# Optimization experiments

Hardware: AMD Instinct MI355X
Metric: run time of the kernel (lower is better)

The kernel has to match this reference:

```python
import jax, jax.numpy as jnp
import numpy as np
import math

N, E = 10000, 640000
IN, HID, OUT, EF = 64, 64, 64, 16


def setup_inputs() -> dict:
    key = jax.random.key(0)
    ks = jax.random.split(key, 16)
    def lin(k, fan_in, fan_out):
        return jax.random.normal(k, (fan_in, fan_out), jnp.float32) / np.sqrt(fan_in)
    return {
        "node_feat": jax.random.normal(ks[0], (N, IN), jnp.float32),
        "coord_feat": jax.random.normal(ks[1], (N, 3), jnp.float32),
        "edge_feat": jax.random.normal(ks[2], (E, EF), jnp.float32),
        "W_e1": lin(ks[3], 2 * IN + EF + 1, HID), "b_e1": jnp.zeros((HID,), jnp.float32),
        "W_e2": lin(ks[4], HID, HID), "b_e2": jnp.zeros((HID,), jnp.float32),
        "W_n1": lin(ks[5], IN + HID, HID), "b_n1": jnp.zeros((HID,), jnp.float32),
        "W_n2": lin(ks[6], HID, OUT), "b_n2": jnp.zeros((OUT,), jnp.float32),
        "W_q": lin(ks[7], IN, HID),
        "W_k": lin(ks[8], IN + EF + 1, HID),
        "src": jax.random.randint(ks[9], (E,), 0, N, jnp.int32),
        "dst": jax.random.randint(ks[10], (E,), 0, N, jnp.int32),
    }


def reference(node_feat, coord_feat, edge_feat,
              W_e1, b_e1, W_e2, b_e2, W_n1, b_n1, W_n2, b_n2,
              W_q, W_k, src, dst):
    silu = jax.nn.silu
    # per-edge gathers
    h_src = node_feat[src]                      # [E, IN]
    h_dst = node_feat[dst]                      # [E, IN]
    x_diff = coord_feat[src] - coord_feat[dst]  # [E, 3]
    dist = jnp.sqrt(jnp.sum(x_diff * x_diff, axis=1, keepdims=True))  # [E, 1]
    # edge MLP message
    f = jnp.concatenate([h_src, h_dst, dist, edge_feat], axis=-1)      # [E, 2*IN+1+EF]
    msg_h = silu(silu(f @ W_e1 + b_e1) @ W_e2 + b_e2)                  # [E, HID]
    # attention score (QK dot)
    k_raw = jnp.concatenate([h_src, dist, edge_feat], axis=-1)         # [E, IN+1+EF]
    msg_k = k_raw @ W_k                                                # [E, HID]
    msg_q = h_dst @ W_q                                                # [E, HID]
    e = jnp.sum(msg_k * msg_q, axis=-1) / math.sqrt(HID)               # [E]
    # segment softmax over incoming edges of each dst node
    e_max = jax.ops.segment_max(e, dst, num_segments=N)                # [N]
    e_exp = jnp.exp(e - e_max[dst])                                    # [E]
    denom = jax.ops.segment_sum(e_exp, dst, num_segments=N)            # [N]
    att = e_exp / denom[dst]                                           # [E]
    # attention-weighted scatter-sum aggregation
    h_neigh = jax.ops.segment_sum(msg_h * att[:, None], dst, num_segments=N)  # [N, HID]
    # node MLP
    h = silu(jnp.concatenate([node_feat, h_neigh], axis=-1) @ W_n1 + b_n1) @ W_n2 + b_n2
    return h
```

## Files before the change

kernel.cpp:

```cpp
#include <hip/hip_runtime.h>

#define NN 10000
#define NE 640000

typedef __attribute__((ext_vector_type(8))) short bf16x8;
typedef __attribute__((ext_vector_type(4))) short s16x4;
typedef __attribute__((ext_vector_type(4))) float f32x4;

#define MFMA __builtin_amdgcn_mfma_f32_16x16x32_bf16

static __device__ __forceinline__ float silu_f(float x) {
    return x / (1.f + __expf(-x));
}
static __device__ __forceinline__ float silu_fast(float x) {
    float d = 1.f + __expf(-x);
    float r; asm("v_rcp_f32 %0, %1" : "=v"(r) : "v"(d));
    return x * r;
}
static __device__ __forceinline__ short f2bf(float x) {
    union { float f; unsigned u; } v; v.f = x;
    unsigned r = (v.u + 0x7FFF + ((v.u >> 16) & 1)) >> 16;
    return (short)r;
}
static __device__ __forceinline__ float bf2f(short h) {
    union { float f; unsigned u; } v; v.u = ((unsigned)(unsigned short)h) << 16;
    return v.f;
}

__global__ __launch_bounds__(256) void k_hist(const int* __restrict__ dst,
                                              int* __restrict__ cnt) {
    int e = blockIdx.x * 256 + threadIdx.x;
    if (e < NE) atomicAdd(&cnt[dst[e]], 1);
}

__global__ __launch_bounds__(256) void k_scan(const int* __restrict__ cnt,
                                              int* __restrict__ row_start,
                                              int* __restrict__ cursor) {
    __shared__ int sv[NN];
    __shared__ int part[256];
    __shared__ int base[257];
    const int t = threadIdx.x;
    for (int i = t; i < NN; i += 256) sv[i] = cnt[i];
    __syncthreads();
    int s = 0;
    #pragma unroll
    for (int i = 0; i < 40; i++) {
        int idx = t * 40 + i;
        int v = (idx < NN) ? sv[idx] : 0;
        if (idx < NN) sv[idx] = s;
        s += v;
    }
    part[t] = s;
    __syncthreads();
    if (t == 0) {
        int a = 0;
        for (int j = 0; j < 256; j++) { base[j] = a; a += part[j]; }
        base[256] = a;
    }
    __syncthreads();
    for (int i = t; i < NN; i += 256) {
        int v = base[i / 40] + sv[i];
        row_start[i] = v; cursor[i] = v;
    }
    if (t == 0) row_start[NN] = base[256];
}

__global__ __launch_bounds__(256) void k_scatter(const int* __restrict__ dst,
                                                 int* __restrict__ cursor,
                                                 int* __restrict__ perm) {
    int e = blockIdx.x * 256 + threadIdx.x;
    if (e < NE) {
        int d = dst[e];
        int p = atomicAdd(&cursor[d], 1);
        perm[p] = e;
    }
}

__global__ __launch_bounds__(256) void k_pack(
    const int* __restrict__ perm, const int* __restrict__ src,
    const int* __restrict__ dst, const float* __restrict__ ef,
    const float* __restrict__ coord,
    int* __restrict__ src_s, unsigned short* __restrict__ dist_s,
    unsigned short* __restrict__ efs)
{
    int p = blockIdx.x * 256 + threadIdx.x;
    if (p >= NE) return;
    const int e = perm[p];
    const int s = src[e];
    const int d = dst[e];

    const float dx = coord[s*3+0] - coord[d*3+0];
    const float dy = coord[s*3+1] - coord[d*3+1];
    const float dz = coord[s*3+2] - coord[d*3+2];
    const float dist = sqrtf(dx*dx + dy*dy + dz*dz);

    src_s[p] = s;
    dist_s[p] = (unsigned short)f2bf(dist);

    const float4* ep = (const float4*)(ef + (size_t)e*16);
    #pragma unroll
    for (int j = 0; j < 4; j++) {
        float4 a = ep[j];
        s16x4 p4;
        p4[0] = f2bf(a.x); p4[1] = f2bf(a.y); p4[2] = f2bf(a.z); p4[3] = f2bf(a.w);
        *(s16x4*)&efs[(size_t)p*16 + j*4] = p4;
    }
}

__global__ __launch_bounds__(256) void node_pre_kernel(
    const float* __restrict__ node_feat,
    const float* __restrict__ W_e1,
    const float* __restrict__ W_k,
    const float* __restrict__ W_q,
    short* __restrict__ nfb, float* __restrict__ B,
    float* __restrict__ G, float* __restrict__ EQn, float* __restrict__ WQn)
{
    __shared__ float sW1b[64*64];
    __shared__ float sWq[64*64];
    __shared__ float sWk[64*65];
    __shared__ float sWke[16*65];
    __shared__ __align__(16) float sx[4][64];
    __shared__ __align__(16) float sq[4][64];

    for (int i = threadIdx.x; i < 64*64; i += 256) {
        sW1b[i] = W_e1[64*64 + i];
        sWq[i]  = W_q[i];
        int c = i >> 6, j = i & 63;
        sWk[c*65 + j] = W_k[i];
    }
    for (int i = threadIdx.x; i < 16*64; i += 256) {
        int k = i >> 6, j = i & 63;
        sWke[k*65 + j] = W_k[(65 + k)*64 + j];
    }
    __syncthreads();

    const int wid = threadIdx.x >> 6;
    const int lane = threadIdx.x & 63;
    for (int n = blockIdx.x * 4 + wid; n < NN; n += gridDim.x * 4) {
        float x = node_feat[n*64 + lane];
        nfb[n*64 + lane] = f2bf(x);
        sx[wid][lane] = x;
        float b = 0.f, q = 0.f;
        #pragma unroll
        for (int i = 0; i < 64; i += 4) {
            float4 x4 = *(const float4*)&sx[wid][i];
            b += x4.x*sW1b[(i+0)*64+lane] + x4.y*sW1b[(i+1)*64+lane]
               + x4.z*sW1b[(i+2)*64+lane] + x4.w*sW1b[(i+3)*64+lane];
            q += x4.x*sWq[(i+0)*64+lane] + x4.y*sWq[(i+1)*64+lane]
               + x4.z*sWq[(i+2)*64+lane] + x4.w*sWq[(i+3)*64+lane];
        }
        B[n*64 + lane] = b;
        sq[wid][lane] = q;

        float g = 0.f;
        #pragma unroll
        for (int j = 0; j < 64; j += 4) {
            float4 q4 = *(const float4*)&sq[wid][j];
            g += q4.x*sWk[lane*65 + j]   + q4.y*sWk[lane*65 + j+1]
               + q4.z*sWk[lane*65 + j+2] + q4.w*sWk[lane*65 + j+3];
        }
        G[n*64 + lane] = g;

        float p = W_k[64*64 + lane] * q;
        #pragma unroll
        for (int off = 32; off; off >>= 1) p += __shfl_xor(p, off);
        if (lane == 0) WQn[n] = p;

        int kk = lane & 15, pp = lane >> 4;
        float s = 0.f;
        #pragma unroll
        for (int jj = 0; jj < 16; jj++) {
            int j = pp*16 + jj;
            s += sWke[kk*65 + j] * sq[wid][j];
        }
        s += __shfl_xor(s, 16); s += __shfl_xor(s, 32);
        if (lane < 16) EQn[n*16 + kk] = s;
    }
}

__global__ __launch_bounds__(512, 2) void edge_kernel(
    const short* __restrict__ nfb, const int* __restrict__ src_s,
    const unsigned short* __restrict__ dist_s,
    const unsigned short* __restrict__ efs, const int* __restrict__ row_start,
    const float* __restrict__ W_e1, const float* __restrict__ b_e1,
    const float* __restrict__ W_e2, const float* __restrict__ b_e2,
    const float* __restrict__ B, const float* __restrict__ G,
    const float* __restrict__ EQn, const float* __restrict__ WQn,
    float* __restrict__ hout)
{
    __shared__ short sW1T[64*104];
    __shared__ short sW2T[64*72];
    __shared__ short sX[8][16*104];
    __shared__ short sH1[8][16*72];
    __shared__ __align__(16) float sG[8][64];
    __shared__ __align__(16) float sEQ[8][16];

    const int tid = threadIdx.x;
    const int wid = tid >> 6, l = tid & 63;
    const int cl = l & 15, rg = l >> 4;
    const int er = l >> 2, q = l & 3;

    for (int i = tid; i < 64*104; i += 512) sW1T[i] = 0;
    __syncthreads();
    for (int i = tid; i < 64*82; i += 512) {
        int k = i >> 6, c = i & 63;
        float v;
        if (k < 64)       v = W_e1[k*64 + c];
        else if (k < 80)  v = W_e1[(129 + k - 64)*64 + c];
        else if (k == 80) v = W_e1[128*64 + c];
        else              v = b_e1[c];
        int s = (c & 3) * 16 + (c >> 2);
        sW1T[s*104 + k] = f2bf(v);
    }
    for (int i = tid; i < 64*64; i += 512) {
        int k = i >> 6, c = i & 63;
        int s = (c & 3) * 16 + (c >> 2);
        sW2T[s*72 + k] = f2bf(W_e2[k*64 + c]);
    }
    if (l < 16) {
        #pragma unroll
        for (int c = 82; c < 96; c++) sX[wid][l*104 + c] = 0;
        sX[wid][l*104 + 81] = (short)0x3F80;
    }
    __syncthreads();

    const int n = blockIdx.x * 8 + wid;
    const int beg = row_start[n], end = row_start[n+1];

    const size_t nb = (size_t)n*64;
    const float4 Bb4 = *(const float4*)&B[nb + cl*4];
    const float4 b24 = *(const float4*)&b_e2[cl*4];
    sG[wid][l] = G[nb + l];
    if (l < 16) sEQ[wid][l] = EQn[(size_t)n*16 + l];
    const float wq = WQn[n];

    float hs0 = 0.f, hs1 = 0.f, hs2 = 0.f, hs3 = 0.f, den = 0.f;

    int idx = beg + er; if (idx > NE-1) idx = NE-1;
    int sN = src_s[idx];
    bf16x8 nfAN = *(const bf16x8*)&nfb[(size_t)sN*64 + q*8];
    bf16x8 nfBN = *(const bf16x8*)&nfb[(size_t)sN*64 + 32 + q*8];
    s16x4  efN  = *(const s16x4*)&efs[(size_t)idx*16 + q*4];
    unsigned short dN = dist_s[idx];

    for (int c0 = beg; c0 < end; c0 += 16) {
        bf16x8 nfA = nfAN, nfB = nfBN; s16x4 ef4 = efN;
        unsigned short dcur = dN;

        int idx2 = c0 + 16 + er; if (idx2 > NE-1) idx2 = NE-1;
        sN = src_s[idx2];
        nfAN = *(const bf16x8*)&nfb[(size_t)sN*64 + q*8];
        nfBN = *(const bf16x8*)&nfb[(size_t)sN*64 + 32 + q*8];
        efN  = *(const s16x4*)&efs[(size_t)idx2*16 + q*4];
        dN   = dist_s[idx2];

        const float dist = bf2f((short)dcur);
        float p_ = 0.f;
        #pragma unroll
        for (int i = 0; i < 8; i++) {
            p_ += bf2f(nfA[i]) * sG[wid][q*8 + i];
            p_ += bf2f(nfB[i]) * sG[wid][32 + q*8 + i];
        }
        #pragma unroll
        for (int i = 0; i < 4; i++)
            p_ += bf2f(ef4[i]) * sEQ[wid][q*4 + i];
        p_ += __shfl_xor(p_, 1); p_ += __shfl_xor(p_, 2);
        const float wgt = __expf((p_ + dist * wq) * 0.125f);

        *(bf16x8*)&sX[wid][er*104 + q*8]      = nfA;
        *(bf16x8*)&sX[wid][er*104 + 32 + q*8] = nfB;
        *(s16x4*)&sX[wid][er*104 + 64 + q*4]  = ef4;
        if (q == 0) sX[wid][er*104 + 80] = (short)dcur;

        bf16x8 ax0 = *(const bf16x8*)&sX[wid][cl*104 +  0 + rg*8];
        bf16x8 ax1 = *(const bf16x8*)&sX[wid][cl*104 + 32 + rg*8];
        bf16x8 ax2 = *(const bf16x8*)&sX[wid][cl*104 + 64 + rg*8];
        f32x4 a0 = {Bb4.x,Bb4.x,Bb4.x,Bb4.x}, a1 = {Bb4.y,Bb4.y,Bb4.y,Bb4.y};
        f32x4 a2 = {Bb4.z,Bb4.z,Bb4.z,Bb4.z}, a3 = {Bb4.w,Bb4.w,Bb4.w,Bb4.w};
        a0 = MFMA(ax0, *(const bf16x8*)&sW1T[( 0+cl)*104 +  0 + rg*8], a0, 0,0,0);
        a0 = MFMA(ax1, *(const bf16x8*)&sW1T[( 0+cl)*104 + 32 + rg*8], a0, 0,0,0);
        a0 = MFMA(ax2, *(const bf16x8*)&sW1T[( 0+cl)*104 + 64 + rg*8], a0, 0,0,0);
        a1 = MFMA(ax0, *(const bf16x8*)&sW1T[(16+cl)*104 +  0 + rg*8], a1, 0,0,0);
        a1 = MFMA(ax1, *(const bf16x8*)&sW1T[(16+cl)*104 + 32 + rg*8], a1, 0,0,0);
        a1 = MFMA(ax2, *(const bf16x8*)&sW1T[(16+cl)*104 + 64 + rg*8], a1, 0,0,0);
        a2 = MFMA(ax0, *(const bf16x8*)&sW1T[(32+cl)*104 +  0 + rg*8], a2, 0,0,0);
        a2 = MFMA(ax1, *(const bf16x8*)&sW1T[(32+cl)*104 + 32 + rg*8], a2, 0,0,0);
        a2 = MFMA(ax2, *(const bf16x8*)&sW1T[(32+cl)*104 + 64 + rg*8], a2, 0,0,0);
        a3 = MFMA(ax0, *(const bf16x8*)&sW1T[(48+cl)*104 +  0 + rg*8], a3, 0,0,0);
        a3 = MFMA(ax1, *(const bf16x8*)&sW1T[(48+cl)*104 + 32 + rg*8], a3, 0,0,0);
        a3 = MFMA(ax2, *(const bf16x8*)&sW1T[(48+cl)*104 + 64 + rg*8], a3, 0,0,0);
        #pragma unroll
        for (int r = 0; r < 4; r++) {
            int row = rg*4 + r;
            float s0 = silu_fast(a0[r]), s1 = silu_fast(a1[r]);
            float s2 = silu_fast(a2[r]), s3 = silu_fast(a3[r]);
            unsigned lo, hi;
            asm("v_cvt_pk_bf16_f32 %0, %1, %2" : "=v"(lo) : "v"(s0), "v"(s1));
            asm("v_cvt_pk_bf16_f32 %0, %1, %2" : "=v"(hi) : "v"(s2), "v"(s3));
            uint2 u; u.x = lo; u.y = hi;
            *(uint2*)&sH1[wid][row*72 + cl*4] = u;
        }

        bf16x8 ah0 = *(const bf16x8*)&sH1[wid][cl*72 + rg*8];
        bf16x8 ah1 = *(const bf16x8*)&sH1[wid][cl*72 + 32 + rg*8];
        f32x4 c0v = {b24.x,b24.x,b24.x,b24.x}, c1v = {b24.y,b24.y,b24.y,b24.y};
        f32x4 c2v = {b24.z,b24.z,b24.z,b24.z}, c3v = {b24.w,b24.w,b24.w,b24.w};
        c0v = MFMA(ah0, *(const bf16x8*)&sW2T[( 0+cl)*72 +      rg*8], c0v, 0,0,0);
        c0v = MFMA(ah1, *(const bf16x8*)&sW2T[( 0+cl)*72 + 32 + rg*8], c0v, 0,0,0);
        c1v = MFMA(ah0, *(const bf16x8*)&sW2T[(16+cl)*72 +      rg*8], c1v, 0,0,0);
        c1v = MFMA(ah1, *(const bf16x8*)&sW2T[(16+cl)*72 + 32 + rg*8], c1v, 0,0,0);
        c2v = MFMA(ah0, *(const bf16x8*)&sW2T[(32+cl)*72 +      rg*8], c2v, 0,0,0);
        c2v = MFMA(ah1, *(const bf16x8*)&sW2T[(32+cl)*72 + 32 + rg*8], c2v, 0,0,0);
        c3v = MFMA(ah0, *(const bf16x8*)&sW2T[(48+cl)*72 +      rg*8], c3v, 0,0,0);
        c3v = MFMA(ah1, *(const bf16x8*)&sW2T[(48+cl)*72 + 32 + rg*8], c3v, 0,0,0);

        #pragma unroll
        for (int r = 0; r < 4; r++) {
            int row = rg*4 + r;
            float wr = (c0 + row < end) ? __shfl(wgt, row << 2) : 0.f;
            hs0 += wr * silu_fast(c0v[r]);
            hs1 += wr * silu_fast(c1v[r]);
            hs2 += wr * silu_fast(c2v[r]);
            hs3 += wr * silu_fast(c3v[r]);
            den += wr;
        }
    }

    hs0 += __shfl_xor(hs0, 16); hs0 += __shfl_xor(hs0, 32);
    hs1 += __shfl_xor(hs1, 16); hs1 += __shfl_xor(hs1, 32);
    hs2 += __shfl_xor(hs2, 16); hs2 += __shfl_xor(hs2, 32);
    hs3 += __shfl_xor(hs3, 16); hs3 += __shfl_xor(hs3, 32);
    den += __shfl_xor(den, 16); den += __shfl_xor(den, 32);

    float v = (rg == 0) ? hs0 : (rg == 1) ? hs1 : (rg == 2) ? hs2 : hs3;
    hout[nb + cl*4 + rg] = (den > 0.f) ? v / den : 0.f;
}

__global__ __launch_bounds__(256) void node_out_kernel(
    const float* __restrict__ node_feat,
    const float* __restrict__ W_n1, const float* __restrict__ b_n1,
    const float* __restrict__ W_n2, const float* __restrict__ b_n2,
    const float* __restrict__ hacc, float* __restrict__ out)
{
    __shared__ float sWn1[128*64];
    __shared__ float sWn2[64*64];
    __shared__ __align__(16) float sx[4][64], sg[4][64], st[4][64];

    for (int i = threadIdx.x; i < 128*64; i += 256) sWn1[i] = W_n1[i];
    for (int i = threadIdx.x; i < 64*64; i += 256)  sWn2[i] = W_n2[i];
    __syncthreads();

    const int wid = threadIdx.x >> 6;
    const int lane = threadIdx.x & 63;
    for (int n = blockIdx.x * 4 + wid; n < NN; n += gridDim.x * 4) {
        sx[wid][lane] = node_feat[n*64 + lane];
        sg[wid][lane] = hacc[n*64 + lane];

        float acc = b_n1[lane];
        #pragma unroll
        for (int i = 0; i < 64; i += 4) {
            float4 x4 = *(const float4*)&sx[wid][i];
            float4 g4 = *(const float4*)&sg[wid][i];
            acc += x4.x*sWn1[(i+0)*64+lane] + x4.y*sWn1[(i+1)*64+lane]
                 + x4.z*sWn1[(i+2)*64+lane] + x4.w*sWn1[(i+3)*64+lane];
            acc += g4.x*sWn1[(64+i+0)*64+lane] + g4.y*sWn1[(64+i+1)*64+lane]
                 + g4.z*sWn1[(64+i+2)*64+lane] + g4.w*sWn1[(64+i+3)*64+lane];
        }
        const float tt = silu_f(acc);
        st[wid][lane] = tt;

        float acc2 = b_n2[lane];
        #pragma unroll
        for (int i = 0; i < 64; i += 4) {
            float4 t4 = *(const float4*)&st[wid][i];
            acc2 += t4.x*sWn2[(i+0)*64+lane] + t4.y*sWn2[(i+1)*64+lane]
                  + t4.z*sWn2[(i+2)*64+lane] + t4.w*sWn2[(i+3)*64+lane];
        }
        out[n*64 + lane] = acc2;
    }
}

extern "C" void kernel_launch(void* const* d_in, const int* in_sizes, int n_in,
                              void* d_out, int out_size, void* d_ws, size_t ws_size,
                              hipStream_t stream) {
    const float* node_feat = (const float*)d_in[0];
    const float* coord     = (const float*)d_in[1];
    const float* edge_feat = (const float*)d_in[2];
    const float* W_e1 = (const float*)d_in[3];
    const float* b_e1 = (const float*)d_in[4];
    const float* W_e2 = (const float*)d_in[5];
    const float* b_e2 = (const float*)d_in[6];
    const float* W_n1 = (const float*)d_in[7];
    const float* b_n1 = (const float*)d_in[8];
    const float* W_n2 = (const float*)d_in[9];
    const float* b_n2 = (const float*)d_in[10];
    const float* W_q  = (const float*)d_in[11];
    const float* W_k  = (const float*)d_in[12];
    const int* src = (const int*)d_in[13];
    const int* dst = (const int*)d_in[14];
    float* out = (float*)d_out;

    float* ws = (float*)d_ws;
    short* nfb       = (short*)ws;
    float* B         = ws + 320000;
    float* G         = ws + 960000;
    float* EQn       = ws + 1600000;
    float* WQn       = ws + 1760000;
    int*   cnt       = (int*)(ws + 1770000);
    int*   row_start = (int*)(ws + 1780000);
    int*   cursor    = (int*)(ws + 1790004);
    int*   perm      = (int*)(ws + 1800004);
    int*   src_s     = (int*)(ws + 2440004);
    unsigned short* dist_s = (unsigned short*)(ws + 3080004);
    unsigned short* efs    = (unsigned short*)(ws + 3400004);
    float* hacc      = ws + 8520004;

    hipMemsetAsync(cnt, 0, NN * sizeof(int), stream);

    node_pre_kernel<<<2500, 256, 0, stream>>>(node_feat, W_e1, W_k, W_q,
                                              nfb, B, G, EQn, WQn);
    k_hist<<<2500, 256, 0, stream>>>(dst, cnt);
    k_scan<<<1, 256, 0, stream>>>(cnt, row_start, cursor);
    k_scatter<<<2500, 256, 0, stream>>>(dst, cursor, perm);
    k_pack<<<2500, 256, 0, stream>>>(perm, src, dst, edge_feat, coord,
                                     src_s, dist_s, efs);
    edge_kernel<<<1250, 512, 0, stream>>>(nfb, src_s, dist_s, efs, row_start,
                                          W_e1, b_e1, W_e2, b_e2,
                                          B, G, EQn, WQn, hacc);
    node_out_kernel<<<2500, 256, 0, stream>>>(node_feat, W_n1, b_n1, W_n2, b_n2,
                                              hacc, out);
}
```

Baseline: 348.2 us.

## Feed gathered edge operands straight to MFMA and pipeline the two MLP layers

The edge kernel no longer stages gathered node and edge features through an LDS buffer. Each lane loads its slice directly in the MFMA operand layout, and the attention dot product now uses the same registers. The second MLP layer for the previous 16-edge chunk runs alongside the first layer of the current chunk, with the hidden tile carried in LDS and one extra drain iteration. The kernel also becomes a persistent grid-stride loop over nodes, with a higher occupancy hint and smaller grids for several kernels. This cuts LDS traffic and exposes overlap, at the cost of more registers and a risk that the smaller grids for the other kernels only work if those kernels loop over nodes.

```diff
diff --git a/kernel.cpp b/kernel.cpp
--- a/kernel.cpp
+++ b/kernel.cpp
@@ -178,7 +178,7 @@
     }
 }
 
-__global__ __launch_bounds__(512, 2) void edge_kernel(
+__global__ __launch_bounds__(512, 4) void edge_kernel(
     const short* __restrict__ nfb, const int* __restrict__ src_s,
     const unsigned short* __restrict__ dist_s,
     const unsigned short* __restrict__ efs, const int* __restrict__ row_start,
@@ -190,15 +190,12 @@
 {
     __shared__ short sW1T[64*104];
     __shared__ short sW2T[64*72];
-    __shared__ short sX[8][16*104];
     __shared__ short sH1[8][16*72];
-    __shared__ __align__(16) float sG[8][64];
-    __shared__ __align__(16) float sEQ[8][16];
+    __shared__ __align__(16) float sC[8][96];
 
     const int tid = threadIdx.x;
     const int wid = tid >> 6, l = tid & 63;
     const int cl = l & 15, rg = l >> 4;
-    const int er = l >> 2, q = l & 3;
 
     for (int i = tid; i < 64*104; i += 512) sW1T[i] = 0;
     __syncthreads();
@@ -217,123 +214,133 @@
         int s = (c & 3) * 16 + (c >> 2);
         sW2T[s*72 + k] = f2bf(W_e2[k*64 + c]);
     }
-    if (l < 16) {
-        #pragma unroll
-        for (int c = 82; c < 96; c++) sX[wid][l*104 + c] = 0;
-        sX[wid][l*104 + 81] = (short)0x3F80;
-    }
-    __syncthreads();
-
-    const int n = blockIdx.x * 8 + wid;
-    const int beg = row_start[n], end = row_start[n+1];
-
-    const size_t nb = (size_t)n*64;
-    const float4 Bb4 = *(const float4*)&B[nb + cl*4];
+    __syncthreads();
+
     const float4 b24 = *(const float4*)&b_e2[cl*4];
-    sG[wid][l] = G[nb + l];
-    if (l < 16) sEQ[wid][l] = EQn[(size_t)n*16 + l];
-    const float wq = WQn[n];
-
-    float hs0 = 0.f, hs1 = 0.f, hs2 = 0.f, hs3 = 0.f, den = 0.f;
-
-    int idx = beg + er; if (idx > NE-1) idx = NE-1;
-    int sN = src_s[idx];
-    bf16x8 nfAN = *(const bf16x8*)&nfb[(size_t)sN*64 + q*8];
-    bf16x8 nfBN = *(const bf16x8*)&nfb[(size_t)sN*64 + 32 + q*8];
-    s16x4  efN  = *(const s16x4*)&efs[(size_t)idx*16 + q*4];
-    unsigned short dN = dist_s[idx];
-
-    for (int c0 = beg; c0 < end; c0 += 16) {
-        bf16x8 nfA = nfAN, nfB = nfBN; s16x4 ef4 = efN;
-        unsigned short dcur = dN;
-
-        int idx2 = c0 + 16 + er; if (idx2 > NE-1) idx2 = NE-1;
-        sN = src_s[idx2];
-        nfAN = *(const bf16x8*)&nfb[(size_t)sN*64 + q*8];
-        nfBN = *(const bf16x8*)&nfb[(size_t)sN*64 + 32 + q*8];
-        efN  = *(const s16x4*)&efs[(size_t)idx2*16 + q*4];
-        dN   = dist_s[idx2];
-
-        const float dist = bf2f((short)dcur);
-        float p_ = 0.f;
-        #pragma unroll
-        for (int i = 0; i < 8; i++) {
-            p_ += bf2f(nfA[i]) * sG[wid][q*8 + i];
-            p_ += bf2f(nfB[i]) * sG[wid][32 + q*8 + i];
-        }
-        #pragma unroll
-        for (int i = 0; i < 4; i++)
-            p_ += bf2f(ef4[i]) * sEQ[wid][q*4 + i];
-        p_ += __shfl_xor(p_, 1); p_ += __shfl_xor(p_, 2);
-        const float wgt = __expf((p_ + dist * wq) * 0.125f);
-
-        *(bf16x8*)&sX[wid][er*104 + q*8]      = nfA;
-        *(bf16x8*)&sX[wid][er*104 + 32 + q*8] = nfB;
-        *(s16x4*)&sX[wid][er*104 + 64 + q*4]  = ef4;
-        if (q == 0) sX[wid][er*104 + 80] = (short)dcur;
-
-        bf16x8 ax0 = *(const bf16x8*)&sX[wid][cl*104 +  0 + rg*8];
-        bf16x8 ax1 = *(const bf16x8*)&sX[wid][cl*104 + 32 + rg*8];
-        bf16x8 ax2 = *(const bf16x8*)&sX[wid][cl*104 + 64 + rg*8];
-        f32x4 a0 = {Bb4.x,Bb4.x,Bb4.x,Bb4.x}, a1 = {Bb4.y,Bb4.y,Bb4.y,Bb4.y};
-        f32x4 a2 = {Bb4.z,Bb4.z,Bb4.z,Bb4.z}, a3 = {Bb4.w,Bb4.w,Bb4.w,Bb4.w};
-        a0 = MFMA(ax0, *(const bf16x8*)&sW1T[( 0+cl)*104 +  0 + rg*8], a0, 0,0,0);
-        a0 = MFMA(ax1, *(const bf16x8*)&sW1T[( 0+cl)*104 + 32 + rg*8], a0, 0,0,0);
-        a0 = MFMA(ax2, *(const bf16x8*)&sW1T[( 0+cl)*104 + 64 + rg*8], a0, 0,0,0);
-        a1 = MFMA(ax0, *(const bf16x8*)&sW1T[(16+cl)*104 +  0 + rg*8], a1, 0,0,0);
-        a1 = MFMA(ax1, *(const bf16x8*)&sW1T[(16+cl)*104 + 32 + rg*8], a1, 0,0,0);
-        a1 = MFMA(ax2, *(const bf16x8*)&sW1T[(16+cl)*104 + 64 + rg*8], a1, 0,0,0);
-        a2 = MFMA(ax0, *(const bf16x8*)&sW1T[(32+cl)*104 +  0 + rg*8], a2, 0,0,0);
-        a2 = MFMA(ax1, *(const bf16x8*)&sW1T[(32+cl)*104 + 32 + rg*8], a2, 0,0,0);
-        a2 = MFMA(ax2, *(const bf16x8*)&sW1T[(32+cl)*104 + 64 + rg*8], a2, 0,0,0);
-        a3 = MFMA(ax0, *(const bf16x8*)&sW1T[(48+cl)*104 +  0 + rg*8], a3, 0,0,0);
-        a3 = MFMA(ax1, *(const bf16x8*)&sW1T[(48+cl)*104 + 32 + rg*8], a3, 0,0,0);
-        a3 = MFMA(ax2, *(const bf16x8*)&sW1T[(48+cl)*104 + 64 + rg*8], a3, 0,0,0);
-        #pragma unroll
-        for (int r = 0; r < 4; r++) {
-            int row = rg*4 + r;
-            float s0 = silu_fast(a0[r]), s1 = silu_fast(a1[r]);
-            float s2 = silu_fast(a2[r]), s3 = silu_fast(a3[r]);
-            unsigned lo, hi;
-            asm("v_cvt_pk_bf16_f32 %0, %1, %2" : "=v"(lo) : "v"(s0), "v"(s1));
-            asm("v_cvt_pk_bf16_f32 %0, %1, %2" : "=v"(hi) : "v"(s2), "v"(s3));
-            uint2 u; u.x = lo; u.y = hi;
-            *(uint2*)&sH1[wid][row*72 + cl*4] = u;
-        }
-
-        bf16x8 ah0 = *(const bf16x8*)&sH1[wid][cl*72 + rg*8];
-        bf16x8 ah1 = *(const bf16x8*)&sH1[wid][cl*72 + 32 + rg*8];
-        f32x4 c0v = {b24.x,b24.x,b24.x,b24.x}, c1v = {b24.y,b24.y,b24.y,b24.y};
-        f32x4 c2v = {b24.z,b24.z,b24.z,b24.z}, c3v = {b24.w,b24.w,b24.w,b24.w};
-        c0v = MFMA(ah0, *(const bf16x8*)&sW2T[( 0+cl)*72 +      rg*8], c0v, 0,0,0);
-        c0v = MFMA(ah1, *(const bf16x8*)&sW2T[( 0+cl)*72 + 32 + rg*8], c0v, 0,0,0);
-        c1v = MFMA(ah0, *(const bf16x8*)&sW2T[(16+cl)*72 +      rg*8], c1v, 0,0,0);
-        c1v = MFMA(ah1, *(const bf16x8*)&sW2T[(16+cl)*72 + 32 + rg*8], c1v, 0,0,0);
-        c2v = MFMA(ah0, *(const bf16x8*)&sW2T[(32+cl)*72 +      rg*8], c2v, 0,0,0);
-        c2v = MFMA(ah1, *(const bf16x8*)&sW2T[(32+cl)*72 + 32 + rg*8], c2v, 0,0,0);
-        c3v = MFMA(ah0, *(const bf16x8*)&sW2T[(48+cl)*72 +      rg*8], c3v, 0,0,0);
-        c3v = MFMA(ah1, *(const bf16x8*)&sW2T[(48+cl)*72 + 32 + rg*8], c3v, 0,0,0);
-
-        #pragma unroll
-        for (int r = 0; r < 4; r++) {
-            int row = rg*4 + r;
-            float wr = (c0 + row < end) ? __shfl(wgt, row << 2) : 0.f;
-            hs0 += wr * silu_fast(c0v[r]);
-            hs1 += wr * silu_fast(c1v[r]);
-            hs2 += wr * silu_fast(c2v[r]);
-            hs3 += wr * silu_fast(c3v[r]);
-            den += wr;
-        }
-    }
-
-    hs0 += __shfl_xor(hs0, 16); hs0 += __shfl_xor(hs0, 32);
-    hs1 += __shfl_xor(hs1, 16); hs1 += __shfl_xor(hs1, 32);
-    hs2 += __shfl_xor(hs2, 16); hs2 += __shfl_xor(hs2, 32);
-    hs3 += __shfl_xor(hs3, 16); hs3 += __shfl_xor(hs3, 32);
-    den += __shfl_xor(den, 16); den += __shfl_xor(den, 32);
-
-    float v = (rg == 0) ? hs0 : (rg == 1) ? hs1 : (rg == 2) ? hs2 : hs3;
-    hout[nb + cl*4 + rg] = (den > 0.f) ? v / den : 0.f;
+
+    for (int n = blockIdx.x * 8 + wid; n < NN; n += gridDim.x * 8) {
+        const int beg = row_start[n], end = row_start[n+1];
+        const size_t nb = (size_t)n*64;
+        const float4 Bb4 = *(const float4*)&B[nb + cl*4];
+
+        sC[wid][l] = G[nb + l];
+        if (l < 16) sC[wid][64 + l] = EQn[(size_t)n*16 + l];
+        if (l == 16) sC[wid][80] = WQn[n];
+        if (l >= 17 && l < 32) sC[wid][64 + l] = 0.f;
+
+        {
+            unsigned* hp = (unsigned*)&sH1[wid][0];
+            #pragma unroll
+            for (int i = l; i < 576; i += 64) hp[i] = 0u;
+        }
+
+        float hs0 = 0.f, hs1 = 0.f, hs2 = 0.f, hs3 = 0.f, den = 0.f;
+        float w_prev = 0.f;
+
+        bf16x8 pA, pB, pE;
+        #pragma unroll
+        for (int i = 0; i < 8; i++) pE[i] = 0;
+        unsigned short pD = 0;
+        {
+            int idx = beg + cl; if (idx > NE-1) idx = NE-1;
+            int sN = src_s[idx];
+            pA = *(const bf16x8*)&nfb[(size_t)sN*64 + rg*8];
+            pB = *(const bf16x8*)&nfb[(size_t)sN*64 + 32 + rg*8];
+            if (rg < 2)       pE = *(const bf16x8*)&efs[(size_t)idx*16 + rg*8];
+            else if (rg == 2) pD = dist_s[idx];
+        }
+
+        for (int c0 = beg; c0 < end + 16; c0 += 16) {
+            bf16x8 ah0 = *(const bf16x8*)&sH1[wid][cl*72 + rg*8];
+            bf16x8 ah1 = *(const bf16x8*)&sH1[wid][cl*72 + 32 + rg*8];
+
+            bf16x8 ax0 = pA, ax1 = pB, pEc = pE;
+            unsigned short pDc = pD;
+
+            {
+                int idx2 = c0 + 16 + cl; if (idx2 > NE-1) idx2 = NE-1;
+                int sN = src_s[idx2];
+                pA = *(const bf16x8*)&nfb[(size_t)sN*64 + rg*8];
+                pB = *(const bf16x8*)&nfb[(size_t)sN*64 + 32 + rg*8];
+                if (rg < 2)       pE = *(const bf16x8*)&efs[(size_t)idx2*16 + rg*8];
+                else if (rg == 2) pD = dist_s[idx2];
+            }
+
+            bf16x8 ax2;
+            #pragma unroll
+            for (int i = 0; i < 8; i++) ax2[i] = 0;
+            if (rg < 2) ax2 = pEc;
+            else if (rg == 2) { ax2[0] = (short)pDc; ax2[1] = (short)0x3F80; }
+
+            f32x4 a0 = {Bb4.x,Bb4.x,Bb4.x,Bb4.x}, a1 = {Bb4.y,Bb4.y,Bb4.y,Bb4.y};
+            f32x4 a2 = {Bb4.z,Bb4.z,Bb4.z,Bb4.z}, a3 = {Bb4.w,Bb4.w,Bb4.w,Bb4.w};
+            a0 = MFMA(ax0, *(const bf16x8*)&sW1T[( 0+cl)*104 +  0 + rg*8], a0, 0,0,0);
+            a0 = MFMA(ax1, *(const bf16x8*)&sW1T[( 0+cl)*104 + 32 + rg*8], a0, 0,0,0);
+            a0 = MFMA(ax2, *(const bf16x8*)&sW1T[( 0+cl)*104 + 64 + rg*8], a0, 0,0,0);
+            a1 = MFMA(ax0, *(const bf16x8*)&sW1T[(16+cl)*104 +  0 + rg*8], a1, 0,0,0);
+            a1 = MFMA(ax1, *(const bf16x8*)&sW1T[(16+cl)*104 + 32 + rg*8], a1, 0,0,0);
+            a1 = MFMA(ax2, *(const bf16x8*)&sW1T[(16+cl)*104 + 64 + rg*8], a1, 0,0,0);
+            a2 = MFMA(ax0, *(const bf16x8*)&sW1T[(32+cl)*104 +  0 + rg*8], a2, 0,0,0);
+            a2 = MFMA(ax1, *(const bf16x8*)&sW1T[(32+cl)*104 + 32 + rg*8], a2, 0,0,0);
+            a2 = MFMA(ax2, *(const bf16x8*)&sW1T[(32+cl)*104 + 64 + rg*8], a2, 0,0,0);
+            a3 = MFMA(ax0, *(const bf16x8*)&sW1T[(48+cl)*104 +  0 + rg*8], a3, 0,0,0);
+            a3 = MFMA(ax1, *(const bf16x8*)&sW1T[(48+cl)*104 + 32 + rg*8], a3, 0,0,0);
+            a3 = MFMA(ax2, *(const bf16x8*)&sW1T[(48+cl)*104 + 64 + rg*8], a3, 0,0,0);
+
+            f32x4 c0v = {b24.x,b24.x,b24.x,b24.x}, c1v = {b24.y,b24.y,b24.y,b24.y};
+            f32x4 c2v = {b24.z,b24.z,b24.z,b24.z}, c3v = {b24.w,b24.w,b24.w,b24.w};
+            c0v = MFMA(ah0, *(const bf16x8*)&sW2T[( 0+cl)*72 +      rg*8], c0v, 0,0,0);
+            c0v = MFMA(ah1, *(const bf16x8*)&sW2T[( 0+cl)*72 + 32 + rg*8], c0v, 0,0,0);
+            c1v = MFMA(ah0, *(const bf16x8*)&sW2T[(16+cl)*72 +      rg*8], c1v, 0,0,0);
+            c1v = MFMA(ah1, *(const bf16x8*)&sW2T[(16+cl)*72 + 32 + rg*8], c1v, 0,0,0);
+            c2v = MFMA(ah0, *(const bf16x8*)&sW2T[(32+cl)*72 +      rg*8], c2v, 0,0,0);
+            c2v = MFMA(ah1, *(const bf16x8*)&sW2T[(32+cl)*72 + 32 + rg*8], c2v, 0,0,0);
+            c3v = MFMA(ah0, *(const bf16x8*)&sW2T[(48+cl)*72 +      rg*8], c3v, 0,0,0);
+            c3v = MFMA(ah1, *(const bf16x8*)&sW2T[(48+cl)*72 + 32 + rg*8], c3v, 0,0,0);
+
+            float p_ = 0.f;
+            #pragma unroll
+            for (int i = 0; i < 8; i++) {
+                p_ += bf2f(ax0[i]) * sC[wid][rg*8 + i];
+                p_ += bf2f(ax1[i]) * sC[wid][32 + rg*8 + i];
+                p_ += bf2f(ax2[i]) * sC[wid][64 + rg*8 + i];
+            }
+            p_ += __shfl_xor(p_, 16); p_ += __shfl_xor(p_, 32);
+            float wgt = (c0 + cl < end) ? __expf(p_ * 0.125f) : 0.f;
+
+            #pragma unroll
+            for (int r = 0; r < 4; r++) {
+                int row = rg*4 + r;
+                float s0 = silu_fast(a0[r]), s1 = silu_fast(a1[r]);
+                float s2 = silu_fast(a2[r]), s3 = silu_fast(a3[r]);
+                unsigned lo, hi;
+                asm("v_cvt_pk_bf16_f32 %0, %1, %2" : "=v"(lo) : "v"(s0), "v"(s1));
+                asm("v_cvt_pk_bf16_f32 %0, %1, %2" : "=v"(hi) : "v"(s2), "v"(s3));
+                uint2 u; u.x = lo; u.y = hi;
+                *(uint2*)&sH1[wid][row*72 + cl*4] = u;
+            }
+
+            #pragma unroll
+            for (int r = 0; r < 4; r++) {
+                float wr = __shfl(w_prev, rg*4 + r);
+                hs0 += wr * silu_fast(c0v[r]);
+                hs1 += wr * silu_fast(c1v[r]);
+                hs2 += wr * silu_fast(c2v[r]);
+                hs3 += wr * silu_fast(c3v[r]);
+                den += wr;
+            }
+            w_prev = wgt;
+        }
+
+        hs0 += __shfl_xor(hs0, 16); hs0 += __shfl_xor(hs0, 32);
+        hs1 += __shfl_xor(hs1, 16); hs1 += __shfl_xor(hs1, 32);
+        hs2 += __shfl_xor(hs2, 16); hs2 += __shfl_xor(hs2, 32);
+        hs3 += __shfl_xor(hs3, 16); hs3 += __shfl_xor(hs3, 32);
+        den += __shfl_xor(den, 16); den += __shfl_xor(den, 32);
+
+        float v = (rg == 0) ? hs0 : (rg == 1) ? hs1 : (rg == 2) ? hs2 : hs3;
+        hout[nb + cl*4 + rg] = (den > 0.f) ? v / den : 0.f;
+    }
 }
 
 __global__ __launch_bounds__(256) void node_out_kernel(
@@ -417,16 +424,16 @@
 
     hipMemsetAsync(cnt, 0, NN * sizeof(int), stream);
 
-    node_pre_kernel<<<2500, 256, 0, stream>>>(node_feat, W_e1, W_k, W_q,
-                                              nfb, B, G, EQn, WQn);
+    node_pre_kernel<<<320, 256, 0, stream>>>(node_feat, W_e1, W_k, W_q,
+                                             nfb, B, G, EQn, WQn);
     k_hist<<<2500, 256, 0, stream>>>(dst, cnt);
     k_scan<<<1, 256, 0, stream>>>(cnt, row_start, cursor);
     k_scatter<<<2500, 256, 0, stream>>>(dst, cursor, perm);
     k_pack<<<2500, 256, 0, stream>>>(perm, src, dst, edge_feat, coord,
                                      src_s, dist_s, efs);
-    edge_kernel<<<1250, 512, 0, stream>>>(nfb, src_s, dist_s, efs, row_start,
-                                          W_e1, b_e1, W_e2, b_e2,
-                                          B, G, EQn, WQn, hacc);
-    node_out_kernel<<<2500, 256, 0, stream>>>(node_feat, W_n1, b_n1, W_n2, b_n2,
-                                              hacc, out);
-}
+    edge_kernel<<<625, 512, 0, stream>>>(nfb, src_s, dist_s, efs, row_start,
+                                         W_e1, b_e1, W_e2, b_e2,
+                                         B, G, EQn, WQn, hacc);
+    node_out_kernel<<<320, 256, 0, stream>>>(node_feat, W_n1, b_n1, W_n2, b_n2,
+                                             hacc, out);
+}
```

Measured after the change: 613.5 us. +76.2%, slower.
